# Optimization experiments

Measured on AMD Instinct MI355X. Metric: run time of the kernel, lower is better.

Reference implementation:

```python
import jax, jax.numpy as jnp
import numpy as np

N, E, F, R, S = 20000, 320000, 64, 8, 10
AVG_NEIGH = 16.0


def setup_inputs() -> dict:
    key = jax.random.key(0)
    ks = jax.random.split(key, 16)
    inp = {
        "vectors": jax.random.normal(ks[0], (E, 3), jnp.float32),
        "node_feats": jax.random.normal(ks[1], (N, F, 4), jnp.float32),  # [N, F, 1(0e)+3(1o)]
        "node_specie": jax.random.randint(ks[2], (N,), 0, S),
        "radial_embedding": jax.random.normal(ks[3], (E, R), jnp.float32),
        "senders": jax.random.randint(ks[4], (E,), 0, N),
        "receivers": jax.random.randint(ks[5], (E,), 0, N),
        # residual FullyConnectedTensorProduct(feats, one-hot species 0e) == species-dep. linear per l
        "W_res_s": jax.random.normal(ks[6], (S, F, F), jnp.float32),
        "W_res_v": jax.random.normal(ks[7], (S, F, F), jnp.float32),
        # interaction block: input linear per l
        "W_in_s": jax.random.normal(ks[8], (F, F), jnp.float32),
        "W_in_v": jax.random.normal(ks[9], (F, F), jnp.float32),
        # radial MLP -> 5 CG tensor-product path weights per channel
        "mlp_w1": jax.random.normal(ks[10], (R, 64), jnp.float32),
        "mlp_w2": jax.random.normal(ks[11], (64, 5 * F), jnp.float32) / 8.0,
        # interaction block: output linear per l
        "W_out_s": jax.random.normal(ks[12], (F, F), jnp.float32),
        "W_out_v": jax.random.normal(ks[13], (F, F), jnp.float32),
        # symmetric product basis (correlation 3), species-dependent term weights
        "W_prod_s": jax.random.normal(ks[14], (S, 5, F), jnp.float32) * 0.3,
        "W_prod_v": jax.random.normal(ks[15], (S, 4, F), jnp.float32) * 0.3,
    }
    k2 = jax.random.split(jax.random.key(1), 3)
    inp["W_lin_s"] = jax.random.normal(k2[0], (F, F), jnp.float32)
    inp["W_lin_v"] = jax.random.normal(k2[1], (F, F), jnp.float32)
    inp["W_read"] = jax.random.normal(k2[2], (F, 1), jnp.float32)
    return inp


def _forward(vectors, node_feats, node_specie, radial_embedding, senders, receivers,
             W_res_s, W_res_v, W_in_s, W_in_v, mlp_w1, mlp_w2, W_out_s, W_out_v,
             W_prod_s, W_prod_v, W_lin_s, W_lin_v, W_read):
    inv_sf = 1.0 / jnp.sqrt(jnp.float32(F))
    s = node_feats[..., 0]          # [N,F]   0e channels
    v = node_feats[..., 1:]         # [N,F,3] 1o channels

    # --- residual connection: FCTP(feats, one-hot species 0e attrs) -> species-gated linear per l
    res_s = jnp.einsum('nf,ngf->ng', s, W_res_s[node_specie]) * inv_sf
    res_v = jnp.einsum('nfc,ngf->ngc', v, W_res_v[node_specie]) * inv_sf

    # --- InteractionBlock ---
    h_s = (s @ W_in_s) * inv_sf
    h_v = jnp.einsum('nfc,fg->ngc', v, W_in_v) * inv_sf

    # spherical harmonics up to max_ell=1: Y0 = 1, Y1 = unit edge vector
    r = jnp.sqrt(jnp.sum(vectors * vectors, -1) + 1e-12)
    Y1 = vectors / r[:, None]                                # [E,3]

    # radial MLP produces per-edge weights for the 5 CG paths:
    # (0e x Y0 -> 0e), (1o . Y1 -> 0e), (0e x Y1 -> 1o), (1o x Y0 -> 1o), (1o x Y1 -> 1o, cross)
    w = (jax.nn.silu(radial_embedding @ mlp_w1) @ mlp_w2).reshape(-1, 5, F)  # [E,5,F]

    ss = h_s[senders]                                        # [E,F]
    sv = h_v[senders]                                        # [E,F,3]
    dot = jnp.einsum('efc,ec->ef', sv, Y1)                   # [E,F]
    m_s = w[:, 0] * ss + w[:, 1] * dot                       # [E,F]
    m_v = (w[:, 2] * ss)[:, :, None] * Y1[:, None, :] \
        + w[:, 3][:, :, None] * sv \
        + w[:, 4][:, :, None] * jnp.cross(sv, Y1[:, None, :])  # [E,F,3]

    agg_s = jnp.zeros_like(h_s).at[receivers].add(m_s) / AVG_NEIGH
    agg_v = jnp.zeros_like(h_v).at[receivers].add(m_v) / AVG_NEIGH
    a_s = (agg_s @ W_out_s) * inv_sf
    a_v = jnp.einsum('nfc,fg->ngc', agg_v, W_out_v) * inv_sf

    # --- EquivariantProductBasisBlock: correlation-3 symmetric contraction, species-dependent ---
    vv = jnp.sum(a_v * a_v, -1)                              # [N,F] invariant |v|^2
    Wp = W_prod_s[node_specie]                               # [N,5,F]
    p_s = (Wp[:, 0] * a_s + Wp[:, 1] * a_s ** 2 + Wp[:, 2] * a_s ** 3
           + Wp[:, 3] * vv + Wp[:, 4] * a_s * vv)
    Wv = W_prod_v[node_specie]                               # [N,4,F]
    p_v = (Wv[:, 0] + Wv[:, 1] * a_s + Wv[:, 2] * a_s ** 2 + Wv[:, 3] * vv)[:, :, None] * a_v

    f_s = (p_s @ W_lin_s) * inv_sf + res_s
    f_v = jnp.einsum('nfc,fg->ngc', p_v, W_lin_v) * inv_sf + res_v

    # --- LinearReadoutBlock (output_irreps = 0e), 1 head ---
    node_out = ((f_s @ W_read) * inv_sf)[:, None, :]         # [N, heads=1, 1]
    new_feats = jnp.concatenate([f_s[..., None], f_v], axis=-1)  # [N,F,4]
    return node_out, new_feats


def reference(vectors, node_feats, node_specie, radial_embedding, senders, receivers,
              W_res_s, W_res_v, W_in_s, W_in_v, mlp_w1, mlp_w2, W_out_s, W_out_v,
              W_prod_s, W_prod_v, W_lin_s, W_lin_v, W_read):
    return _forward(vectors, node_feats, node_specie, radial_embedding, senders, receivers,
                    W_res_s, W_res_v, W_in_s, W_in_v, mlp_w1, mlp_w2, W_out_s, W_out_v,
                    W_prod_s, W_prod_v, W_lin_s, W_lin_v, W_read)
```

## Files before the change

### kernel.cpp

```cpp
#include <hip/hip_runtime.h>
#include <math.h>

#define NN 20000
#define NE 320000
#define NF (NN*64)
#define TB 16

__device__ __forceinline__ float silu_f(float x){ return x / (1.0f + expf(-x)); }

__global__ __launch_bounds__(256) void k_transpose_res(
    const float* __restrict__ Ws, const float* __restrict__ Wv,
    float* __restrict__ Wst, float* __restrict__ Wvt)
{
  int i = blockIdx.x*256 + threadIdx.x;
  int spec = i >> 12;
  int g = (i >> 6) & 63;
  int f = i & 63;
  Wst[spec*4096 + f*64 + g] = Ws[i];
  Wvt[spec*4096 + f*64 + g] = Wv[i];
}

__global__ __launch_bounds__(256) void k_node_pre(
    const float* __restrict__ node_feats, const float* __restrict__ W_in_s,
    const float* __restrict__ W_in_v, float* __restrict__ h_s, float* __restrict__ h_v)
{
  __shared__ float sh[4][4][64];
  int wave = threadIdx.x >> 6, lane = threadIdx.x & 63;
  int n = blockIdx.x*4 + wave;
  int o = n*64 + lane;
  float4 nf = *(const float4*)(node_feats + (size_t)o*4);
  sh[wave][0][lane]=nf.x; sh[wave][1][lane]=nf.y; sh[wave][2][lane]=nf.z; sh[wave][3][lane]=nf.w;
  __syncthreads();
  float as=0.f, av0=0.f, av1=0.f, av2=0.f;
  #pragma unroll 8
  for(int f=0; f<64; ++f){
    float ws = W_in_s[f*64+lane], wv = W_in_v[f*64+lane];
    as  += sh[wave][0][f]*ws;
    av0 += sh[wave][1][f]*wv;
    av1 += sh[wave][2][f]*wv;
    av2 += sh[wave][3][f]*wv;
  }
  h_s[o]      = as *0.125f;
  h_v[o]      = av0*0.125f;
  h_v[NF+o]   = av1*0.125f;
  h_v[2*NF+o] = av2*0.125f;
}

__global__ __launch_bounds__(256) void k_edge(
    const float* __restrict__ vectors, const float* __restrict__ radial,
    const int* __restrict__ senders, const int* __restrict__ receivers,
    const float* __restrict__ mlp_w1, const float* __restrict__ mlp_w2,
    const float* __restrict__ h_s, const float* __restrict__ h_v,
    float* __restrict__ agg_s, float* __restrict__ agg_v)
{
  __shared__ float rad[4][128];
  __shared__ float hid[4][TB][64];
  int wave = threadIdx.x >> 6, lane = threadIdx.x & 63;
  int wgid = blockIdx.x*4 + wave;
  int e0 = wgid*TB;
  rad[wave][lane]    = radial[e0*8 + lane];
  rad[wave][64+lane] = radial[e0*8 + 64 + lane];
  __syncthreads();
  #pragma unroll
  for(int t=0;t<TB;++t){
    float acc=0.f;
    #pragma unroll
    for(int r=0;r<8;++r) acc += rad[wave][t*8+r]*mlp_w1[r*64+lane];
    hid[wave][t][lane] = silu_f(acc);
  }
  __syncthreads();
  float w[5][TB];
  #pragma unroll
  for(int j=0;j<5;++j)
    #pragma unroll
    for(int t=0;t<TB;++t) w[j][t]=0.f;
  for(int h=0; h<64; h+=2){
    float b0[5], b1[5];
    #pragma unroll
    for(int j=0;j<5;++j){
      b0[j]=mlp_w2[h*320     + j*64 + lane];
      b1[j]=mlp_w2[(h+1)*320 + j*64 + lane];
    }
    #pragma unroll
    for(int t=0;t<TB;++t){
      float2 hb = *(const float2*)&hid[wave][t][h];
      #pragma unroll
      for(int j=0;j<5;++j) w[j][t] = fmaf(hb.x, b0[j], fmaf(hb.y, b1[j], w[j][t]));
    }
  }
  #pragma unroll
  for(int t=0;t<TB;++t){
    int e = e0 + t;
    int snd = senders[e], rcv = receivers[e];
    float vx=vectors[e*3], vy=vectors[e*3+1], vz=vectors[e*3+2];
    float rinv = 1.0f/sqrtf(vx*vx+vy*vy+vz*vz+1e-12f);
    float y0=vx*rinv, y1=vy*rinv, y2=vz*rinv;
    int so = snd*64+lane, ro = rcv*64+lane;
    float ss  = h_s[so];
    float sv0 = h_v[so], sv1 = h_v[NF+so], sv2 = h_v[2*NF+so];
    float dot = sv0*y0 + sv1*y1 + sv2*y2;
    float ms  = w[0][t]*ss + w[1][t]*dot;
    float w2s = w[2][t]*ss, w3t = w[3][t], w4t = w[4][t];
    float mv0 = w2s*y0 + w3t*sv0 + w4t*(sv1*y2 - sv2*y1);
    float mv1 = w2s*y1 + w3t*sv1 + w4t*(sv2*y0 - sv0*y2);
    float mv2 = w2s*y2 + w3t*sv2 + w4t*(sv0*y1 - sv1*y0);
    atomicAdd(&agg_s[ro],      ms);
    atomicAdd(&agg_v[ro],      mv0);
    atomicAdd(&agg_v[NF+ro],   mv1);
    atomicAdd(&agg_v[2*NF+ro], mv2);
  }
}

__global__ __launch_bounds__(256) void k_node_post(
  const float* __restrict__ node_feats, const int* __restrict__ specie,
  const float* __restrict__ agg_s, const float* __restrict__ agg_v,
  const float* __restrict__ Wrst, const float* __restrict__ Wrvt,
  const float* __restrict__ W_out_s, const float* __restrict__ W_out_v,
  const float* __restrict__ W_prod_s, const float* __restrict__ W_prod_v,
  const float* __restrict__ W_lin_s, const float* __restrict__ W_lin_v,
  const float* __restrict__ W_read, float* __restrict__ out_node, float* __restrict__ out_feats)
{
  __shared__ float shA[4][4][64];
  __shared__ float shS[4][4][64];
  __shared__ float shP[4][4][64];
  int wave = threadIdx.x >> 6, lane = threadIdx.x & 63;
  int n = blockIdx.x*4 + wave;
  int o = n*64 + lane;
  shA[wave][0][lane] = agg_s[o]      * (1.f/16.f);
  shA[wave][1][lane] = agg_v[o]      * (1.f/16.f);
  shA[wave][2][lane] = agg_v[NF+o]   * (1.f/16.f);
  shA[wave][3][lane] = agg_v[2*NF+o] * (1.f/16.f);
  float4 nf = *(const float4*)(node_feats + (size_t)o*4);
  shS[wave][0][lane]=nf.x; shS[wave][1][lane]=nf.y; shS[wave][2][lane]=nf.z; shS[wave][3][lane]=nf.w;
  __syncthreads();
  int spec = specie[n];
  const float* Ws_ = Wrst + spec*4096;
  const float* Wv_ = Wrvt + spec*4096;
  float a_s=0.f,a0=0.f,a1=0.f,a2=0.f, r_s=0.f,r0=0.f,r1=0.f,r2=0.f;
  #pragma unroll 4
  for(int f=0; f<64; ++f){
    float wos=W_out_s[f*64+lane], wov=W_out_v[f*64+lane];
    a_s += shA[wave][0][f]*wos;
    a0  += shA[wave][1][f]*wov;
    a1  += shA[wave][2][f]*wov;
    a2  += shA[wave][3][f]*wov;
    float wrs=Ws_[f*64+lane], wrv=Wv_[f*64+lane];
    r_s += shS[wave][0][f]*wrs;
    r0  += shS[wave][1][f]*wrv;
    r1  += shS[wave][2][f]*wrv;
    r2  += shS[wave][3][f]*wrv;
  }
  a_s*=0.125f; a0*=0.125f; a1*=0.125f; a2*=0.125f;
  r_s*=0.125f; r0*=0.125f; r1*=0.125f; r2*=0.125f;
  float vv = a0*a0 + a1*a1 + a2*a2;
  float as2 = a_s*a_s;
  const float* Wp = W_prod_s + spec*320;
  float p_s = Wp[lane]*a_s + Wp[64+lane]*as2 + Wp[128+lane]*as2*a_s
            + Wp[192+lane]*vv + Wp[256+lane]*a_s*vv;
  const float* Wq = W_prod_v + spec*256;
  float coef = Wq[lane] + Wq[64+lane]*a_s + Wq[128+lane]*as2 + Wq[192+lane]*vv;
  shP[wave][0][lane] = p_s;
  shP[wave][1][lane] = coef*a0;
  shP[wave][2][lane] = coef*a1;
  shP[wave][3][lane] = coef*a2;
  __syncthreads();
  float fs=0.f,f0=0.f,f1=0.f,f2=0.f;
  #pragma unroll 4
  for(int f=0; f<64; ++f){
    float wls=W_lin_s[f*64+lane], wlv=W_lin_v[f*64+lane];
    fs += shP[wave][0][f]*wls;
    f0 += shP[wave][1][f]*wlv;
    f1 += shP[wave][2][f]*wlv;
    f2 += shP[wave][3][f]*wlv;
  }
  fs = fs*0.125f + r_s;
  f0 = f0*0.125f + r0;
  f1 = f1*0.125f + r1;
  f2 = f2*0.125f + r2;
  float x = fs * W_read[lane];
  #pragma unroll
  for(int off=32; off; off>>=1) x += __shfl_down(x, off);
  if(lane==0) out_node[n] = x*0.125f;
  float4 o4; o4.x=fs; o4.y=f0; o4.z=f1; o4.w=f2;
  *(float4*)(out_feats + (size_t)o*4) = o4;
}

extern "C" void kernel_launch(void* const* d_in, const int* in_sizes, int n_in,
                              void* d_out, int out_size, void* d_ws, size_t ws_size,
                              hipStream_t stream) {
  const float* vectors    = (const float*)d_in[0];
  const float* node_feats = (const float*)d_in[1];
  const int*   node_specie= (const int*)  d_in[2];
  const float* radial     = (const float*)d_in[3];
  const int*   senders    = (const int*)  d_in[4];
  const int*   receivers  = (const int*)  d_in[5];
  const float* W_res_s    = (const float*)d_in[6];
  const float* W_res_v    = (const float*)d_in[7];
  const float* W_in_s     = (const float*)d_in[8];
  const float* W_in_v     = (const float*)d_in[9];
  const float* mlp_w1     = (const float*)d_in[10];
  const float* mlp_w2     = (const float*)d_in[11];
  const float* W_out_s    = (const float*)d_in[12];
  const float* W_out_v    = (const float*)d_in[13];
  const float* W_prod_s   = (const float*)d_in[14];
  const float* W_prod_v   = (const float*)d_in[15];
  const float* W_lin_s    = (const float*)d_in[16];
  const float* W_lin_v    = (const float*)d_in[17];
  const float* W_read     = (const float*)d_in[18];

  float* ws   = (float*)d_ws;
  float* h_s  = ws;
  float* h_v  = ws + NF;
  float* agg_s= ws + 4*(size_t)NF;
  float* agg_v= ws + 5*(size_t)NF;
  float* Wrst = ws + 8*(size_t)NF;
  float* Wrvt = ws + 8*(size_t)NF + 40960;

  hipMemsetAsync(agg_s, 0, (size_t)4*NF*sizeof(float), stream);
  k_transpose_res<<<160, 256, 0, stream>>>(W_res_s, W_res_v, Wrst, Wrvt);
  k_node_pre<<<NN/4, 256, 0, stream>>>(node_feats, W_in_s, W_in_v, h_s, h_v);
  k_edge<<<NE/(4*TB), 256, 0, stream>>>(vectors, radial, senders, receivers,
                                        mlp_w1, mlp_w2, h_s, h_v, agg_s, agg_v);
  k_node_post<<<NN/4, 256, 0, stream>>>(node_feats, node_specie, agg_s, agg_v,
                                        Wrst, Wrvt, W_out_s, W_out_v,
                                        W_prod_s, W_prod_v, W_lin_s, W_lin_v,
                                        W_read, (float*)d_out, (float*)d_out + NN);
}
```

Before: 499.1 us.

## Sort edges by receiver, interleave node layout, and batch four nodes per wave

```diff
diff --git a/kernel.cpp b/kernel.cpp
--- a/kernel.cpp
+++ b/kernel.cpp
@@ -5,8 +5,6 @@
 #define NE 320000
 #define NF (NN*64)
 #define TB 16
-
-__device__ __forceinline__ float silu_f(float x){ return x / (1.0f + expf(-x)); }
 
 __global__ __launch_bounds__(256) void k_transpose_res(
     const float* __restrict__ Ws, const float* __restrict__ Wv,
@@ -20,169 +18,272 @@
   Wvt[spec*4096 + f*64 + g] = Wv[i];
 }
 
+__global__ __launch_bounds__(256) void k_hist(const int* __restrict__ receivers,
+                                              int* __restrict__ count)
+{
+  int e = blockIdx.x*256 + threadIdx.x;
+  atomicAdd(&count[receivers[e]], 1);
+}
+
+__global__ __launch_bounds__(256) void k_scan(const int* __restrict__ count,
+                                              int* __restrict__ offset)
+{
+  __shared__ int part[256];
+  int t = threadIdx.x;
+  const int PER = 79;
+  int s = 0;
+  for(int i=0;i<PER;++i){ int idx = t*PER+i; if(idx < NN) s += count[idx]; }
+  part[t] = s;
+  __syncthreads();
+  for(int off=1; off<256; off<<=1){
+    int v = (t>=off) ? part[t-off] : 0;
+    __syncthreads();
+    part[t] += v;
+    __syncthreads();
+  }
+  int run = t ? part[t-1] : 0;
+  for(int i=0;i<PER;++i){
+    int idx = t*PER+i;
+    if(idx < NN){ offset[idx] = run; run += count[idx]; }
+  }
+  if(t==255) offset[NN] = run;
+}
+
+__global__ __launch_bounds__(256) void k_scatter(
+    const int* __restrict__ receivers, const int* __restrict__ offset,
+    int* __restrict__ count, int* __restrict__ order)
+{
+  int e = blockIdx.x*256 + threadIdx.x;
+  int r = receivers[e];
+  int old = atomicSub(&count[r], 1);
+  order[offset[r] + old - 1] = e;
+}
+
 __global__ __launch_bounds__(256) void k_node_pre(
     const float* __restrict__ node_feats, const float* __restrict__ W_in_s,
-    const float* __restrict__ W_in_v, float* __restrict__ h_s, float* __restrict__ h_v)
-{
-  __shared__ float sh[4][4][64];
+    const float* __restrict__ W_in_v, float* __restrict__ h)
+{
+  __shared__ float sh[16][4][64];
   int wave = threadIdx.x >> 6, lane = threadIdx.x & 63;
-  int n = blockIdx.x*4 + wave;
-  int o = n*64 + lane;
-  float4 nf = *(const float4*)(node_feats + (size_t)o*4);
-  sh[wave][0][lane]=nf.x; sh[wave][1][lane]=nf.y; sh[wave][2][lane]=nf.z; sh[wave][3][lane]=nf.w;
-  __syncthreads();
-  float as=0.f, av0=0.f, av1=0.f, av2=0.f;
-  #pragma unroll 8
+  int nb = blockIdx.x*16 + wave*4;
+  #pragma unroll
+  for(int k=0;k<4;++k){
+    int nd = wave*4 + k;
+    float4 nf = *(const float4*)(node_feats + (size_t)((nb+k)*64 + lane)*4);
+    sh[nd][0][lane]=nf.x; sh[nd][1][lane]=nf.y; sh[nd][2][lane]=nf.z; sh[nd][3][lane]=nf.w;
+  }
+  __syncthreads();
+  float as[4]={0,0,0,0}, a0[4]={0,0,0,0}, a1[4]={0,0,0,0}, a2[4]={0,0,0,0};
   for(int f=0; f<64; ++f){
     float ws = W_in_s[f*64+lane], wv = W_in_v[f*64+lane];
-    as  += sh[wave][0][f]*ws;
-    av0 += sh[wave][1][f]*wv;
-    av1 += sh[wave][2][f]*wv;
-    av2 += sh[wave][3][f]*wv;
-  }
-  h_s[o]      = as *0.125f;
-  h_v[o]      = av0*0.125f;
-  h_v[NF+o]   = av1*0.125f;
-  h_v[2*NF+o] = av2*0.125f;
+    #pragma unroll
+    for(int k=0;k<4;++k){
+      int nd = wave*4 + k;
+      as[k] = fmaf(sh[nd][0][f], ws, as[k]);
+      a0[k] = fmaf(sh[nd][1][f], wv, a0[k]);
+      a1[k] = fmaf(sh[nd][2][f], wv, a1[k]);
+      a2[k] = fmaf(sh[nd][3][f], wv, a2[k]);
+    }
+  }
+  #pragma unroll
+  for(int k=0;k<4;++k){
+    size_t o = (size_t)(nb+k)*256 + lane;
+    h[o]     = as[k]*0.125f;
+    h[o+64]  = a0[k]*0.125f;
+    h[o+128] = a1[k]*0.125f;
+    h[o+192] = a2[k]*0.125f;
+  }
 }
 
 __global__ __launch_bounds__(256) void k_edge(
     const float* __restrict__ vectors, const float* __restrict__ radial,
     const int* __restrict__ senders, const int* __restrict__ receivers,
     const float* __restrict__ mlp_w1, const float* __restrict__ mlp_w2,
-    const float* __restrict__ h_s, const float* __restrict__ h_v,
-    float* __restrict__ agg_s, float* __restrict__ agg_v)
-{
-  __shared__ float rad[4][128];
+    const float* __restrict__ h, const int* __restrict__ order,
+    float* __restrict__ agg)
+{
+  __shared__ int   eidS[4][TB];
+  __shared__ int   sndS[4][TB];
+  __shared__ int   rcvS[4][TB];
+  __shared__ float vecS[4][3*TB];
+  __shared__ float rad[4][8*TB];
   __shared__ float hid[4][TB][64];
   int wave = threadIdx.x >> 6, lane = threadIdx.x & 63;
-  int wgid = blockIdx.x*4 + wave;
-  int e0 = wgid*TB;
-  rad[wave][lane]    = radial[e0*8 + lane];
-  rad[wave][64+lane] = radial[e0*8 + 64 + lane];
+  int e0 = (blockIdx.x*4 + wave)*TB;
+
+  if(lane < TB){
+    int e = order[e0 + lane];
+    eidS[wave][lane] = e;
+    sndS[wave][lane] = senders[e];
+    rcvS[wave][lane] = receivers[e];
+  }
+  float wl[8];
+  #pragma unroll
+  for(int r=0;r<8;++r) wl[r] = mlp_w1[r*64+lane];
+  __syncthreads();
+  if(lane < 3*TB) vecS[wave][lane] = vectors[(size_t)eidS[wave][lane/3]*3 + lane%3];
+  rad[wave][lane]    = radial[(size_t)eidS[wave][lane>>3]*8     + (lane&7)];
+  rad[wave][64+lane] = radial[(size_t)eidS[wave][8+(lane>>3)]*8 + (lane&7)];
   __syncthreads();
   #pragma unroll
   for(int t=0;t<TB;++t){
-    float acc=0.f;
-    #pragma unroll
-    for(int r=0;r<8;++r) acc += rad[wave][t*8+r]*mlp_w1[r*64+lane];
-    hid[wave][t][lane] = silu_f(acc);
+    float acc = 0.f;
+    #pragma unroll
+    for(int r=0;r<8;++r) acc = fmaf(rad[wave][t*8+r], wl[r], acc);
+    hid[wave][t][lane] = acc / (1.f + __expf(-acc));
   }
   __syncthreads();
   float w[5][TB];
   #pragma unroll
   for(int j=0;j<5;++j)
     #pragma unroll
-    for(int t=0;t<TB;++t) w[j][t]=0.f;
-  for(int h=0; h<64; h+=2){
+    for(int t=0;t<TB;++t) w[j][t] = 0.f;
+  for(int hh=0; hh<64; hh+=2){
     float b0[5], b1[5];
     #pragma unroll
     for(int j=0;j<5;++j){
-      b0[j]=mlp_w2[h*320     + j*64 + lane];
-      b1[j]=mlp_w2[(h+1)*320 + j*64 + lane];
+      b0[j] = mlp_w2[hh*320     + j*64 + lane];
+      b1[j] = mlp_w2[(hh+1)*320 + j*64 + lane];
     }
     #pragma unroll
     for(int t=0;t<TB;++t){
-      float2 hb = *(const float2*)&hid[wave][t][h];
+      float2 hb = *(const float2*)&hid[wave][t][hh];
       #pragma unroll
       for(int j=0;j<5;++j) w[j][t] = fmaf(hb.x, b0[j], fmaf(hb.y, b1[j], w[j][t]));
     }
   }
+  float as_=0.f, av0=0.f, av1=0.f, av2=0.f;
+  int cur = rcvS[wave][0];
   #pragma unroll
   for(int t=0;t<TB;++t){
-    int e = e0 + t;
-    int snd = senders[e], rcv = receivers[e];
-    float vx=vectors[e*3], vy=vectors[e*3+1], vz=vectors[e*3+2];
-    float rinv = 1.0f/sqrtf(vx*vx+vy*vy+vz*vz+1e-12f);
+    int rcv = rcvS[wave][t];
+    if(rcv != cur){
+      size_t ro = (size_t)cur*256 + lane;
+      atomicAdd(&agg[ro],     as_);
+      atomicAdd(&agg[ro+64],  av0);
+      atomicAdd(&agg[ro+128], av1);
+      atomicAdd(&agg[ro+192], av2);
+      as_=0.f; av0=0.f; av1=0.f; av2=0.f;
+      cur = rcv;
+    }
+    int snd = sndS[wave][t];
+    float vx=vecS[wave][t*3], vy=vecS[wave][t*3+1], vz=vecS[wave][t*3+2];
+    float rinv = rsqrtf(vx*vx + vy*vy + vz*vz + 1e-12f);
     float y0=vx*rinv, y1=vy*rinv, y2=vz*rinv;
-    int so = snd*64+lane, ro = rcv*64+lane;
-    float ss  = h_s[so];
-    float sv0 = h_v[so], sv1 = h_v[NF+so], sv2 = h_v[2*NF+so];
+    size_t so = (size_t)snd*256 + lane;
+    float ss  = h[so];
+    float sv0 = h[so+64], sv1 = h[so+128], sv2 = h[so+192];
     float dot = sv0*y0 + sv1*y1 + sv2*y2;
-    float ms  = w[0][t]*ss + w[1][t]*dot;
+    as_ += w[0][t]*ss + w[1][t]*dot;
     float w2s = w[2][t]*ss, w3t = w[3][t], w4t = w[4][t];
-    float mv0 = w2s*y0 + w3t*sv0 + w4t*(sv1*y2 - sv2*y1);
-    float mv1 = w2s*y1 + w3t*sv1 + w4t*(sv2*y0 - sv0*y2);
-    float mv2 = w2s*y2 + w3t*sv2 + w4t*(sv0*y1 - sv1*y0);
-    atomicAdd(&agg_s[ro],      ms);
-    atomicAdd(&agg_v[ro],      mv0);
-    atomicAdd(&agg_v[NF+ro],   mv1);
-    atomicAdd(&agg_v[2*NF+ro], mv2);
-  }
+    av0 += w2s*y0 + w3t*sv0 + w4t*(sv1*y2 - sv2*y1);
+    av1 += w2s*y1 + w3t*sv1 + w4t*(sv2*y0 - sv0*y2);
+    av2 += w2s*y2 + w3t*sv2 + w4t*(sv0*y1 - sv1*y0);
+  }
+  size_t ro = (size_t)cur*256 + lane;
+  atomicAdd(&agg[ro],     as_);
+  atomicAdd(&agg[ro+64],  av0);
+  atomicAdd(&agg[ro+128], av1);
+  atomicAdd(&agg[ro+192], av2);
 }
 
 __global__ __launch_bounds__(256) void k_node_post(
   const float* __restrict__ node_feats, const int* __restrict__ specie,
-  const float* __restrict__ agg_s, const float* __restrict__ agg_v,
+  const float* __restrict__ agg,
   const float* __restrict__ Wrst, const float* __restrict__ Wrvt,
   const float* __restrict__ W_out_s, const float* __restrict__ W_out_v,
   const float* __restrict__ W_prod_s, const float* __restrict__ W_prod_v,
   const float* __restrict__ W_lin_s, const float* __restrict__ W_lin_v,
-  const float* __restrict__ W_read, float* __restrict__ out_node, float* __restrict__ out_feats)
-{
-  __shared__ float shA[4][4][64];
-  __shared__ float shS[4][4][64];
-  __shared__ float shP[4][4][64];
+  const float* __restrict__ W_read, float* __restrict__ out_node,
+  float* __restrict__ out_feats)
+{
+  __shared__ float shA[16][4][64];
+  __shared__ float shS[16][4][64];
   int wave = threadIdx.x >> 6, lane = threadIdx.x & 63;
-  int n = blockIdx.x*4 + wave;
-  int o = n*64 + lane;
-  shA[wave][0][lane] = agg_s[o]      * (1.f/16.f);
-  shA[wave][1][lane] = agg_v[o]      * (1.f/16.f);
-  shA[wave][2][lane] = agg_v[NF+o]   * (1.f/16.f);
-  shA[wave][3][lane] = agg_v[2*NF+o] * (1.f/16.f);
-  float4 nf = *(const float4*)(node_feats + (size_t)o*4);
-  shS[wave][0][lane]=nf.x; shS[wave][1][lane]=nf.y; shS[wave][2][lane]=nf.z; shS[wave][3][lane]=nf.w;
-  __syncthreads();
-  int spec = specie[n];
-  const float* Ws_ = Wrst + spec*4096;
-  const float* Wv_ = Wrvt + spec*4096;
-  float a_s=0.f,a0=0.f,a1=0.f,a2=0.f, r_s=0.f,r0=0.f,r1=0.f,r2=0.f;
-  #pragma unroll 4
+  int nb = blockIdx.x*16 + wave*4;
+  #pragma unroll
+  for(int k=0;k<4;++k){
+    int nd = wave*4 + k;
+    size_t o = (size_t)(nb+k)*256 + lane;
+    shA[nd][0][lane] = agg[o]     * (1.f/16.f);
+    shA[nd][1][lane] = agg[o+64]  * (1.f/16.f);
+    shA[nd][2][lane] = agg[o+128] * (1.f/16.f);
+    shA[nd][3][lane] = agg[o+192] * (1.f/16.f);
+    float4 nf = *(const float4*)(node_feats + (size_t)((nb+k)*64 + lane)*4);
+    shS[nd][0][lane]=nf.x; shS[nd][1][lane]=nf.y; shS[nd][2][lane]=nf.z; shS[nd][3][lane]=nf.w;
+  }
+  int spec[4];
+  #pragma unroll
+  for(int k=0;k<4;++k) spec[k] = specie[nb+k];
+  __syncthreads();
+  float a_s[4]={0,0,0,0}, a0[4]={0,0,0,0}, a1[4]={0,0,0,0}, a2[4]={0,0,0,0};
+  float r_s[4]={0,0,0,0}, r0[4]={0,0,0,0}, r1[4]={0,0,0,0}, r2[4]={0,0,0,0};
   for(int f=0; f<64; ++f){
-    float wos=W_out_s[f*64+lane], wov=W_out_v[f*64+lane];
-    a_s += shA[wave][0][f]*wos;
-    a0  += shA[wave][1][f]*wov;
-    a1  += shA[wave][2][f]*wov;
-    a2  += shA[wave][3][f]*wov;
-    float wrs=Ws_[f*64+lane], wrv=Wv_[f*64+lane];
-    r_s += shS[wave][0][f]*wrs;
-    r0  += shS[wave][1][f]*wrv;
-    r1  += shS[wave][2][f]*wrv;
-    r2  += shS[wave][3][f]*wrv;
-  }
-  a_s*=0.125f; a0*=0.125f; a1*=0.125f; a2*=0.125f;
-  r_s*=0.125f; r0*=0.125f; r1*=0.125f; r2*=0.125f;
-  float vv = a0*a0 + a1*a1 + a2*a2;
-  float as2 = a_s*a_s;
-  const float* Wp = W_prod_s + spec*320;
-  float p_s = Wp[lane]*a_s + Wp[64+lane]*as2 + Wp[128+lane]*as2*a_s
-            + Wp[192+lane]*vv + Wp[256+lane]*a_s*vv;
-  const float* Wq = W_prod_v + spec*256;
-  float coef = Wq[lane] + Wq[64+lane]*a_s + Wq[128+lane]*as2 + Wq[192+lane]*vv;
-  shP[wave][0][lane] = p_s;
-  shP[wave][1][lane] = coef*a0;
-  shP[wave][2][lane] = coef*a1;
-  shP[wave][3][lane] = coef*a2;
-  __syncthreads();
-  float fs=0.f,f0=0.f,f1=0.f,f2=0.f;
-  #pragma unroll 4
+    float wos = W_out_s[f*64+lane], wov = W_out_v[f*64+lane];
+    #pragma unroll
+    for(int k=0;k<4;++k){
+      int nd = wave*4 + k;
+      a_s[k] = fmaf(shA[nd][0][f], wos, a_s[k]);
+      a0[k]  = fmaf(shA[nd][1][f], wov, a0[k]);
+      a1[k]  = fmaf(shA[nd][2][f], wov, a1[k]);
+      a2[k]  = fmaf(shA[nd][3][f], wov, a2[k]);
+    }
+    #pragma unroll
+    for(int k=0;k<4;++k){
+      int nd = wave*4 + k;
+      float wrs = Wrst[spec[k]*4096 + f*64 + lane];
+      float wrv = Wrvt[spec[k]*4096 + f*64 + lane];
+      r_s[k] = fmaf(shS[nd][0][f], wrs, r_s[k]);
+      r0[k]  = fmaf(shS[nd][1][f], wrv, r0[k]);
+      r1[k]  = fmaf(shS[nd][2][f], wrv, r1[k]);
+      r2[k]  = fmaf(shS[nd][3][f], wrv, r2[k]);
+    }
+  }
+  __syncthreads();
+  #pragma unroll
+  for(int k=0;k<4;++k){
+    int nd = wave*4 + k;
+    float A_s = a_s[k]*0.125f, A0 = a0[k]*0.125f, A1 = a1[k]*0.125f, A2 = a2[k]*0.125f;
+    float vv = A0*A0 + A1*A1 + A2*A2;
+    float as2 = A_s*A_s;
+    const float* Wp = W_prod_s + spec[k]*320;
+    float p_s = Wp[lane]*A_s + Wp[64+lane]*as2 + Wp[128+lane]*as2*A_s
+              + Wp[192+lane]*vv + Wp[256+lane]*A_s*vv;
+    const float* Wq = W_prod_v + spec[k]*256;
+    float coef = Wq[lane] + Wq[64+lane]*A_s + Wq[128+lane]*as2 + Wq[192+lane]*vv;
+    shS[nd][0][lane] = p_s;
+    shS[nd][1][lane] = coef*A0;
+    shS[nd][2][lane] = coef*A1;
+    shS[nd][3][lane] = coef*A2;
+  }
+  __syncthreads();
+  float lfs[4]={0,0,0,0}, lf0[4]={0,0,0,0}, lf1[4]={0,0,0,0}, lf2[4]={0,0,0,0};
   for(int f=0; f<64; ++f){
-    float wls=W_lin_s[f*64+lane], wlv=W_lin_v[f*64+lane];
-    fs += shP[wave][0][f]*wls;
-    f0 += shP[wave][1][f]*wlv;
-    f1 += shP[wave][2][f]*wlv;
-    f2 += shP[wave][3][f]*wlv;
-  }
-  fs = fs*0.125f + r_s;
-  f0 = f0*0.125f + r0;
-  f1 = f1*0.125f + r1;
-  f2 = f2*0.125f + r2;
-  float x = fs * W_read[lane];
-  #pragma unroll
-  for(int off=32; off; off>>=1) x += __shfl_down(x, off);
-  if(lane==0) out_node[n] = x*0.125f;
-  float4 o4; o4.x=fs; o4.y=f0; o4.z=f1; o4.w=f2;
-  *(float4*)(out_feats + (size_t)o*4) = o4;
+    float wls = W_lin_s[f*64+lane], wlv = W_lin_v[f*64+lane];
+    #pragma unroll
+    for(int k=0;k<4;++k){
+      int nd = wave*4 + k;
+      lfs[k] = fmaf(shS[nd][0][f], wls, lfs[k]);
+      lf0[k] = fmaf(shS[nd][1][f], wlv, lf0[k]);
+      lf1[k] = fmaf(shS[nd][2][f], wlv, lf1[k]);
+      lf2[k] = fmaf(shS[nd][3][f], wlv, lf2[k]);
+    }
+  }
+  float wr = W_read[lane];
+  #pragma unroll
+  for(int k=0;k<4;++k){
+    int n = nb + k;
+    float FS = lfs[k]*0.125f + r_s[k]*0.125f;
+    float F0 = lf0[k]*0.125f + r0[k]*0.125f;
+    float F1 = lf1[k]*0.125f + r1[k]*0.125f;
+    float F2 = lf2[k]*0.125f + r2[k]*0.125f;
+    float x = FS * wr;
+    #pragma unroll
+    for(int off=32; off; off>>=1) x += __shfl_down(x, off);
+    if(lane==0) out_node[n] = x*0.125f;
+    float4 o4; o4.x=FS; o4.y=F0; o4.z=F1; o4.w=F2;
+    *(float4*)(out_feats + (size_t)(n*64+lane)*4) = o4;
+  }
 }
 
 extern "C" void kernel_launch(void* const* d_in, const int* in_sizes, int n_in,
@@ -209,20 +310,25 @@
   const float* W_read     = (const float*)d_in[18];
 
   float* ws   = (float*)d_ws;
-  float* h_s  = ws;
-  float* h_v  = ws + NF;
-  float* agg_s= ws + 4*(size_t)NF;
-  float* agg_v= ws + 5*(size_t)NF;
+  float* h    = ws;
+  float* agg  = ws + 4*(size_t)NF;
   float* Wrst = ws + 8*(size_t)NF;
-  float* Wrvt = ws + 8*(size_t)NF + 40960;
-
-  hipMemsetAsync(agg_s, 0, (size_t)4*NF*sizeof(float), stream);
+  float* Wrvt = Wrst + 40960;
+  int*   order  = (int*)(Wrvt + 40960);
+  int*   offset = order + NE;
+  int*   count  = offset + NN + 1;
+
+  hipMemsetAsync(agg,   0, (size_t)4*NF*sizeof(float), stream);
+  hipMemsetAsync(count, 0, (size_t)NN*sizeof(int), stream);
   k_transpose_res<<<160, 256, 0, stream>>>(W_res_s, W_res_v, Wrst, Wrvt);
-  k_node_pre<<<NN/4, 256, 0, stream>>>(node_feats, W_in_s, W_in_v, h_s, h_v);
+  k_hist   <<<NE/256, 256, 0, stream>>>(receivers, count);
+  k_scan   <<<1,      256, 0, stream>>>(count, offset);
+  k_scatter<<<NE/256, 256, 0, stream>>>(receivers, offset, count, order);
+  k_node_pre<<<NN/16, 256, 0, stream>>>(node_feats, W_in_s, W_in_v, h);
   k_edge<<<NE/(4*TB), 256, 0, stream>>>(vectors, radial, senders, receivers,
-                                        mlp_w1, mlp_w2, h_s, h_v, agg_s, agg_v);
-  k_node_post<<<NN/4, 256, 0, stream>>>(node_feats, node_specie, agg_s, agg_v,
-                                        Wrst, Wrvt, W_out_s, W_out_v,
-                                        W_prod_s, W_prod_v, W_lin_s, W_lin_v,
-                                        W_read, (float*)d_out, (float*)d_out + NN);
-}
+                                        mlp_w1, mlp_w2, h, order, agg);
+  k_node_post<<<NN/16, 256, 0, stream>>>(node_feats, node_specie, agg,
+                                         Wrst, Wrvt, W_out_s, W_out_v,
+                                         W_prod_s, W_prod_v, W_lin_s, W_lin_v,
+                                         W_read, (float*)d_out, (float*)d_out + NN);
+}
```

After: 509.3 us. 2.0% more time.
